# Optimization experiments

Hardware: AMD Instinct MI355X
Metric: run time of the kernel (lower is better)

The kernel has to match this reference:

```python
import jax, jax.numpy as jnp
import numpy as np

B, N, DIM = 2, 2048, 512
HEADS, DIM_HEAD = 8, 64
INNER = HEADS * DIM_HEAD  # 512
SCALE = DIM_HEAD ** -0.5


def setup_inputs() -> dict:
    key = jax.random.key(0)
    k1, k2, k3, k4, k5 = jax.random.split(key, 5)
    s = 0.02
    return {
        "x1": jax.random.normal(k1, (B, N, DIM), jnp.float32),
        "x2": jax.random.normal(k2, (B, N, DIM), jnp.float32),
        "W_qk": jax.random.normal(k3, (DIM, 2 * INNER), jnp.float32) * s,
        "W_v": jax.random.normal(k4, (DIM, INNER), jnp.float32) * s,
        "W_out": jax.random.normal(k5, (INNER, DIM), jnp.float32) * s,
        "b_out": jnp.zeros((DIM,), jnp.float32),
    }


def _split_heads(t):
    # [b, n, h*d] -> [b, h, n, d]
    b, n, _ = t.shape
    return t.reshape(b, n, HEADS, DIM_HEAD).transpose(0, 2, 1, 3)


def reference(x1, x2, W_qk, W_v, W_out, b_out):
    # to_qk(x1) -> chunk into k, v ; to_v(x2) -> q  (names in orig are swapped)
    kv = x1 @ W_qk                      # [b, n1, 2*inner]
    k, v = jnp.split(kv, 2, axis=-1)
    q = x2 @ W_v                        # [b, n2, inner]
    q, k, v = _split_heads(q), _split_heads(k), _split_heads(v)  # [b,h,n,d]
    dots = jnp.einsum("bhid,bhjd->bhij", q, k) * SCALE  # [b,h,n2,n1]
    attn = jax.nn.softmax(dots, axis=-1)
    out = jnp.einsum("bhij,bhjd->bhid", attn, v)         # [b,h,n2,d]
    out = out.transpose(0, 2, 1, 3).reshape(out.shape[0], out.shape[2], INNER)
    return out @ W_out + b_out          # [b, n2, dim]
```

## Files before the change

kernel.cpp:

```cpp
#include <hip/hip_runtime.h>

typedef short bf16x8 __attribute__((ext_vector_type(8)));
typedef short bf16x4 __attribute__((ext_vector_type(4)));
typedef float f32x4 __attribute__((ext_vector_type(4)));
typedef float f32x16 __attribute__((ext_vector_type(16)));
typedef unsigned short u16;
typedef u16 u16x8 __attribute__((ext_vector_type(8)));
typedef u16 u16x4 __attribute__((ext_vector_type(4)));

#define DEV __device__ __forceinline__

DEV u16 f2bf(float f) {
  unsigned u = __float_as_uint(f);
  u += 0x7fff + ((u >> 16) & 1);
  return (u16)(u >> 16);
}

DEV int pkbf(float lo, float hi) {
  return __builtin_amdgcn_perm(__float_as_uint(hi) + 0x8000u,
                               __float_as_uint(lo) + 0x8000u, 0x07060302u);
}

#define MFMA16(a, b, c) __builtin_amdgcn_mfma_f32_16x16x32_bf16(a, b, c, 0, 0, 0)
#define MFMA3216(a, b, c) __builtin_amdgcn_mfma_f32_32x32x16_bf16(a, b, c, 0, 0, 0)

#if __has_builtin(__builtin_amdgcn_mfma_f32_32x32x8bf16_1k)
#define HAVE_PV8 1
#define PVMFMA(a, b, c) __builtin_amdgcn_mfma_f32_32x32x8bf16_1k(a, b, c, 0, 0, 0)
#else
#define HAVE_PV8 0
#endif

__global__ __launch_bounds__(256) void wprep(
    const float* __restrict__ Wqk, const float* __restrict__ Wv,
    const float* __restrict__ Wout,
    u16* __restrict__ WqkT, u16* __restrict__ WvT, u16* __restrict__ WoutT) {
  __shared__ float tf[32][33];
  int bx = blockIdx.x, t = threadIdx.x;
  const float* src; u16* dst; int Ncols; int id;
  if (bx < 512)      { id = bx;       src = Wqk;  dst = WqkT;  Ncols = 1024; }
  else if (bx < 768) { id = bx - 512; src = Wv;   dst = WvT;   Ncols = 512; }
  else               { id = bx - 768; src = Wout; dst = WoutT; Ncols = 512; }
  int tilesPerRow = Ncols >> 5;
  int tr = id / tilesPerRow, tc = id % tilesPerRow;
  int r0 = tr * 32, c0 = tc * 32;
  {
    int r = t >> 3, c4 = (t & 7) * 4;
    float4 v = *(const float4*)(src + (long)(r0 + r) * Ncols + c0 + c4);
    tf[r][c4] = v.x; tf[r][c4 + 1] = v.y; tf[r][c4 + 2] = v.z; tf[r][c4 + 3] = v.w;
  }
  __syncthreads();
  {
    int c = t >> 3, r4 = (t & 7) * 4;
    u16x4 o;
    o[0] = f2bf(tf[r4][c]); o[1] = f2bf(tf[r4 + 1][c]);
    o[2] = f2bf(tf[r4 + 2][c]); o[3] = f2bf(tf[r4 + 3][c]);
    *(u16x4*)(dst + (long)(c0 + c) * 512 + r0 + r4) = o;
  }
}

template <int MODE>
__global__ __launch_bounds__(256) void gemm_k(
    const void* __restrict__ Ap, const u16* __restrict__ BT,
    u16* __restrict__ out_q, u16* __restrict__ out_k, u16* __restrict__ out_vt,
    float* __restrict__ out_f, const float* __restrict__ bias) {
  constexpr bool AF32 = (MODE != 2);
  __shared__ u16 sA[2][128 * 40];
  __shared__ u16 sB[2][64 * 40];
  int t = threadIdx.x, bx = blockIdx.x;
  int m0 = (bx & 31) * 128, n0 = (bx >> 5) * 64;
  int w = t >> 6, l = t & 63, lm = l & 15, lq = l >> 4;

  f32x4 zero = {0.f, 0.f, 0.f, 0.f};
  f32x4 acc[2][4];
#pragma unroll
  for (int i = 0; i < 2; ++i)
#pragma unroll
    for (int j = 0; j < 4; ++j) acc[i][j] = zero;

  int sm = t >> 2;
  int skc = (t & 3) * 8;
  const float* gAf = (const float*)Ap + (long)(m0 + sm) * 512 + skc;
  const u16* gAh = (const u16*)Ap + (long)(m0 + sm) * 512 + skc;
  const u16* gB = BT + (long)(n0 + sm) * 512 + skc;

  auto loadA = [&](int kt, int rows) {
    bf16x8 o;
    long off = (long)rows * 512 + kt * 32;
    if constexpr (AF32) {
      float4 f0 = *(const float4*)(gAf + off);
      float4 f1 = *(const float4*)(gAf + off + 4);
      o[0] = (short)f2bf(f0.x); o[1] = (short)f2bf(f0.y);
      o[2] = (short)f2bf(f0.z); o[3] = (short)f2bf(f0.w);
      o[4] = (short)f2bf(f1.x); o[5] = (short)f2bf(f1.y);
      o[6] = (short)f2bf(f1.z); o[7] = (short)f2bf(f1.w);
    } else {
      o = *(const bf16x8*)(gAh + off);
    }
    return o;
  };

  bf16x8 a0 = loadA(0, 0);
  bf16x8 a1 = loadA(0, 64);
  bf16x8 b0 = *(const bf16x8*)(gB);
  *(bf16x8*)(sA[0] + sm * 40 + skc) = a0;
  *(bf16x8*)(sA[0] + (sm + 64) * 40 + skc) = a1;
  *(bf16x8*)(sB[0] + sm * 40 + skc) = b0;
  __syncthreads();

  for (int kt = 0; kt < 16; ++kt) {
    int cur = kt & 1;
    if (kt < 15) {
      a0 = loadA(kt + 1, 0);
      a1 = loadA(kt + 1, 64);
      b0 = *(const bf16x8*)(gB + (kt + 1) * 32);
    }
    bf16x8 af[2], bfr[4];
    af[0] = *(const bf16x8*)(sA[cur] + (w * 32 + lm) * 40 + lq * 8);
    af[1] = *(const bf16x8*)(sA[cur] + (w * 32 + 16 + lm) * 40 + lq * 8);
#pragma unroll
    for (int s = 0; s < 4; ++s)
      bfr[s] = *(const bf16x8*)(sB[cur] + (s * 16 + lm) * 40 + lq * 8);
#pragma unroll
    for (int ms = 0; ms < 2; ++ms)
#pragma unroll
      for (int s = 0; s < 4; ++s)
        acc[ms][s] = MFMA16(af[ms], bfr[s], acc[ms][s]);
    if (kt < 15) {
      int nxt = 1 - cur;
      *(bf16x8*)(sA[nxt] + sm * 40 + skc) = a0;
      *(bf16x8*)(sA[nxt] + (sm + 64) * 40 + skc) = a1;
      *(bf16x8*)(sB[nxt] + sm * 40 + skc) = b0;
    }
    __syncthreads();
  }

#pragma unroll
  for (int ms = 0; ms < 2; ++ms) {
    int gmBase = m0 + w * 32 + ms * 16 + lq * 4;
#pragma unroll
    for (int s = 0; s < 4; ++s) {
      int gc = n0 + s * 16 + lm;
      if (MODE == 2) {
#pragma unroll
        for (int r = 0; r < 4; ++r)
          out_f[(long)(gmBase + r) * 512 + gc] = acc[ms][s][r] + bias[gc];
      } else if (MODE == 0) {
        int b = gmBase >> 11, n = gmBase & 2047;
#pragma unroll
        for (int r = 0; r < 4; ++r)
          out_q[(((long)(b << 3) + (gc >> 6)) * 2048 + n + r) * 64 + (gc & 63)] =
              f2bf(acc[ms][s][r] * 0.125f);
      } else {
        int b = gmBase >> 11, n = gmBase & 2047;
        if (gc < 512) {
#pragma unroll
          for (int r = 0; r < 4; ++r)
            out_k[(((long)(b << 3) + (gc >> 6)) * 2048 + n + r) * 64 + (gc & 63)] =
                f2bf(acc[ms][s][r]);
        } else {
          int c = gc - 512, h = c >> 6, d = c & 63;
          u16x4 vv;
#pragma unroll
          for (int r = 0; r < 4; ++r) vv[r] = f2bf(acc[ms][s][r]);
          *(u16x4*)(out_vt + (((long)(b << 3) + h) * 64 + d) * 2048 + n) = vv;
        }
      }
    }
  }
}

__global__ __launch_bounds__(128) void attn(
    const u16* __restrict__ Q, const u16* __restrict__ K,
    const u16* __restrict__ Vt, u16* __restrict__ O) {
  int id = blockIdx.x;
  int bh = id & 15, qt = id >> 4;
  int b = bh >> 3, h = bh & 7;
  const u16* Kh = K + (long)bh * 2048 * 64;
  const u16* Vh = Vt + (long)bh * 64 * 2048;
  int t = threadIdx.x, w = t >> 6, lane = t & 63, ln = lane & 31, hi = lane >> 5;

  __shared__ u16 sK[2][64 * 72];
  __shared__ u16 sV[2][64 * 72];

  bf16x8 qf[4];
  {
    const u16* qp = Q + (long)bh * 2048 * 64 + (long)(qt * 64 + w * 32 + ln) * 64 + hi * 8;
#pragma unroll
    for (int dc = 0; dc < 4; ++dc) qf[dc] = *(const bf16x8*)(qp + dc * 16);
  }

  f32x16 accO[2];
#pragma unroll
  for (int dt = 0; dt < 2; ++dt)
#pragma unroll
    for (int i = 0; i < 16; ++i) accO[dt][i] = 0.f;
  float dacc = 0.f;

  int r = t >> 1, half = t & 1;
  const u16* gK = Kh + (long)r * 64 + half * 32;
  const u16* gV = Vh + (long)r * 2048 + half * 32;
  int woff = r * 72 + half * 32;

  bf16x8 kp[4], vp[4];
#pragma unroll
  for (int i = 0; i < 4; ++i) {
    kp[i] = *(const bf16x8*)(gK + i * 8);
    vp[i] = *(const bf16x8*)(gV + i * 8);
  }
#pragma unroll
  for (int i = 0; i < 4; ++i) {
    *(bf16x8*)(sK[0] + woff + i * 8) = kp[i];
    *(bf16x8*)(sV[0] + woff + i * 8) = vp[i];
  }
  __syncthreads();

  for (int jt = 0; jt < 32; ++jt) {
    int cur = jt & 1;
    if (jt < 31) {
      long ko = (long)(jt + 1) * 64 * 64, vo = (long)(jt + 1) * 64;
#pragma unroll
      for (int i = 0; i < 4; ++i) {
        kp[i] = *(const bf16x8*)(gK + ko + i * 8);
        vp[i] = *(const bf16x8*)(gV + vo + i * 8);
      }
    }
    const u16* bK = sK[cur];
    const u16* bV = sV[cur];

#pragma unroll
    for (int kt2 = 0; kt2 < 2; ++kt2) {
      f32x16 st;
#pragma unroll
      for (int i = 0; i < 16; ++i) st[i] = 0.f;
#pragma unroll
      for (int dc = 0; dc < 4; ++dc) {
        bf16x8 kf = *(const bf16x8*)(bK + (kt2 * 32 + ln) * 72 + dc * 16 + hi * 8);
        st = MFMA3216(kf, qf[dc], st);
      }
      float p[16];
#pragma unroll
      for (int i = 0; i < 16; ++i) {
        float e = __expf(st[i]);
        p[i] = e;
        dacc += e;
      }
#if HAVE_PV8
#pragma unroll
      for (int c = 0; c < 4; ++c) {
        union { int2 i2; bf16x4 v; } u;
        u.i2.x = pkbf(p[c * 4 + 0], p[c * 4 + 1]);
        u.i2.y = pkbf(p[c * 4 + 2], p[c * 4 + 3]);
#pragma unroll
        for (int dt = 0; dt < 2; ++dt) {
          bf16x4 vf = *(const bf16x4*)(bV + (dt * 32 + ln) * 72 + kt2 * 32 + c * 8 + hi * 4);
          accO[dt] = PVMFMA(vf, u.v, accO[dt]);
        }
      }
#else
#pragma unroll
      for (int c2 = 0; c2 < 2; ++c2) {
        int o0x = pkbf(p[c2 * 8 + 0], p[c2 * 8 + 1]);
        int o0y = pkbf(p[c2 * 8 + 2], p[c2 * 8 + 3]);
        int o1x = pkbf(p[c2 * 8 + 4], p[c2 * 8 + 5]);
        int o1y = pkbf(p[c2 * 8 + 6], p[c2 * 8 + 7]);
        int s0x = __shfl_xor(o0x, 32), s0y = __shfl_xor(o0y, 32);
        int s1x = __shfl_xor(o1x, 32), s1y = __shfl_xor(o1y, 32);
        union { int4 i4; bf16x8 v; } u;
        if (hi) { u.i4.x = s1x; u.i4.y = s1y; u.i4.z = o1x; u.i4.w = o1y; }
        else    { u.i4.x = o0x; u.i4.y = o0y; u.i4.z = s0x; u.i4.w = s0y; }
#pragma unroll
        for (int dt = 0; dt < 2; ++dt) {
          bf16x8 vf = *(const bf16x8*)(bV + (dt * 32 + ln) * 72 + kt2 * 32 + c2 * 16 + hi * 8);
          accO[dt] = MFMA3216(vf, u.v, accO[dt]);
        }
      }
#endif
    }

    if (jt < 31) {
      int nxt = cur ^ 1;
#pragma unroll
      for (int i = 0; i < 4; ++i) {
        *(bf16x8*)(sK[nxt] + woff + i * 8) = kp[i];
        *(bf16x8*)(sV[nxt] + woff + i * 8) = vp[i];
      }
    }
    __syncthreads();
  }

  dacc += __shfl_xor(dacc, 32);
  float inv = 1.f / dacc;

  u16* Ob = O + ((long)b * 2048 + qt * 64 + w * 32 + ln) * 512 + h * 64;
#pragma unroll
  for (int dt = 0; dt < 2; ++dt)
#pragma unroll
    for (int g = 0; g < 4; ++g) {
      u16x4 o;
#pragma unroll
      for (int rr = 0; rr < 4; ++rr) o[rr] = f2bf(accO[dt][g * 4 + rr] * inv);
      *(u16x4*)(Ob + dt * 32 + g * 8 + hi * 4) = o;
    }
}

extern "C" void kernel_launch(void* const* d_in, const int* in_sizes, int n_in,
                              void* d_out, int out_size, void* d_ws, size_t ws_size,
                              hipStream_t stream) {
  const float* x1 = (const float*)d_in[0];
  const float* x2 = (const float*)d_in[1];
  const float* Wqk = (const float*)d_in[2];
  const float* Wv = (const float*)d_in[3];
  const float* Wout = (const float*)d_in[4];
  const float* bout = (const float*)d_in[5];
  float* out = (float*)d_out;

  u16* ws = (u16*)d_ws;
  const long SZ = 2097152;
  u16* Qw = ws;
  u16* Kw = ws + SZ;
  u16* Vtw = ws + 2 * SZ;
  u16* Ow = ws + 3 * SZ;
  u16* WqkT = ws + 4 * SZ;
  u16* WvT = WqkT + 524288;
  u16* WoutT = WvT + 262144;

  wprep<<<1024, 256, 0, stream>>>(Wqk, Wv, Wout, WqkT, WvT, WoutT);
  gemm_k<0><<<256, 256, 0, stream>>>(x2, WvT, Qw, nullptr, nullptr, nullptr, nullptr);
  gemm_k<1><<<512, 256, 0, stream>>>(x1, WqkT, nullptr, Kw, Vtw, nullptr, nullptr);
  attn<<<512, 128, 0, stream>>>(Qw, Kw, Vtw, Ow);
  gemm_k<2><<<256, 256, 0, stream>>>(Ow, WoutT, nullptr, nullptr, nullptr, out, bout);
}
```

Before: 145.3 us.

## Merge Q/KV projection launches, split attention keys across warps, shrink output GEMM tiles

```diff
diff --git a/kernel.cpp b/kernel.cpp
--- a/kernel.cpp
+++ b/kernel.cpp
@@ -59,16 +59,18 @@
   }
 }
 
-template <int MODE>
-__global__ __launch_bounds__(256) void gemm_k(
-    const void* __restrict__ Ap, const u16* __restrict__ BT,
-    u16* __restrict__ out_q, u16* __restrict__ out_k, u16* __restrict__ out_vt,
-    float* __restrict__ out_f, const float* __restrict__ bias) {
-  constexpr bool AF32 = (MODE != 2);
+__global__ __launch_bounds__(256) void qkv_gemm(
+    const float* __restrict__ x1, const float* __restrict__ x2,
+    const u16* __restrict__ WqkT, const u16* __restrict__ WvT,
+    u16* __restrict__ out_q, u16* __restrict__ out_k, u16* __restrict__ out_vt) {
   __shared__ u16 sA[2][128 * 40];
   __shared__ u16 sB[2][64 * 40];
-  int t = threadIdx.x, bx = blockIdx.x;
-  int m0 = (bx & 31) * 128, n0 = (bx >> 5) * 64;
+  int bx = blockIdx.x, t = threadIdx.x;
+  bool isQ = bx < 256;
+  int bx2 = isQ ? bx : bx - 256;
+  const float* Ap = isQ ? x2 : x1;
+  const u16* BT = isQ ? WvT : WqkT;
+  int m0 = (bx2 & 31) * 128, n0 = (bx2 >> 5) * 64;
   int w = t >> 6, l = t & 63, lm = l & 15, lq = l >> 4;
 
   f32x4 zero = {0.f, 0.f, 0.f, 0.f};
@@ -80,23 +82,18 @@
 
   int sm = t >> 2;
   int skc = (t & 3) * 8;
-  const float* gAf = (const float*)Ap + (long)(m0 + sm) * 512 + skc;
-  const u16* gAh = (const u16*)Ap + (long)(m0 + sm) * 512 + skc;
+  const float* gAf = Ap + (long)(m0 + sm) * 512 + skc;
   const u16* gB = BT + (long)(n0 + sm) * 512 + skc;
 
   auto loadA = [&](int kt, int rows) {
+    long off = (long)rows * 512 + kt * 32;
+    float4 f0 = *(const float4*)(gAf + off);
+    float4 f1 = *(const float4*)(gAf + off + 4);
     bf16x8 o;
-    long off = (long)rows * 512 + kt * 32;
-    if constexpr (AF32) {
-      float4 f0 = *(const float4*)(gAf + off);
-      float4 f1 = *(const float4*)(gAf + off + 4);
-      o[0] = (short)f2bf(f0.x); o[1] = (short)f2bf(f0.y);
-      o[2] = (short)f2bf(f0.z); o[3] = (short)f2bf(f0.w);
-      o[4] = (short)f2bf(f1.x); o[5] = (short)f2bf(f1.y);
-      o[6] = (short)f2bf(f1.z); o[7] = (short)f2bf(f1.w);
-    } else {
-      o = *(const bf16x8*)(gAh + off);
-    }
+    o[0] = (short)f2bf(f0.x); o[1] = (short)f2bf(f0.y);
+    o[2] = (short)f2bf(f0.z); o[3] = (short)f2bf(f0.w);
+    o[4] = (short)f2bf(f1.x); o[5] = (short)f2bf(f1.y);
+    o[6] = (short)f2bf(f1.z); o[7] = (short)f2bf(f1.w);
     return o;
   };
 
@@ -141,36 +138,29 @@
 #pragma unroll
     for (int s = 0; s < 4; ++s) {
       int gc = n0 + s * 16 + lm;
-      if (MODE == 2) {
-#pragma unroll
-        for (int r = 0; r < 4; ++r)
-          out_f[(long)(gmBase + r) * 512 + gc] = acc[ms][s][r] + bias[gc];
-      } else if (MODE == 0) {
-        int b = gmBase >> 11, n = gmBase & 2047;
+      int b = gmBase >> 11, n = gmBase & 2047;
+      if (isQ) {
 #pragma unroll
         for (int r = 0; r < 4; ++r)
           out_q[(((long)(b << 3) + (gc >> 6)) * 2048 + n + r) * 64 + (gc & 63)] =
               f2bf(acc[ms][s][r] * 0.125f);
+      } else if (gc < 512) {
+#pragma unroll
+        for (int r = 0; r < 4; ++r)
+          out_k[(((long)(b << 3) + (gc >> 6)) * 2048 + n + r) * 64 + (gc & 63)] =
+              f2bf(acc[ms][s][r]);
       } else {
-        int b = gmBase >> 11, n = gmBase & 2047;
-        if (gc < 512) {
-#pragma unroll
-          for (int r = 0; r < 4; ++r)
-            out_k[(((long)(b << 3) + (gc >> 6)) * 2048 + n + r) * 64 + (gc & 63)] =
-                f2bf(acc[ms][s][r]);
-        } else {
-          int c = gc - 512, h = c >> 6, d = c & 63;
-          u16x4 vv;
-#pragma unroll
-          for (int r = 0; r < 4; ++r) vv[r] = f2bf(acc[ms][s][r]);
-          *(u16x4*)(out_vt + (((long)(b << 3) + h) * 64 + d) * 2048 + n) = vv;
-        }
-      }
-    }
-  }
-}
-
-__global__ __launch_bounds__(128) void attn(
+        int c = gc - 512, h = c >> 6, d = c & 63;
+        u16x4 vv;
+#pragma unroll
+        for (int r = 0; r < 4; ++r) vv[r] = f2bf(acc[ms][s][r]);
+        *(u16x4*)(out_vt + (((long)(b << 3) + h) * 64 + d) * 2048 + n) = vv;
+      }
+    }
+  }
+}
+
+__global__ __launch_bounds__(256, 2) void attn(
     const u16* __restrict__ Q, const u16* __restrict__ K,
     const u16* __restrict__ Vt, u16* __restrict__ O) {
   int id = blockIdx.x;
@@ -179,27 +169,29 @@
   const u16* Kh = K + (long)bh * 2048 * 64;
   const u16* Vh = Vt + (long)bh * 64 * 2048;
   int t = threadIdx.x, w = t >> 6, lane = t & 63, ln = lane & 31, hi = lane >> 5;
-
-  __shared__ u16 sK[2][64 * 72];
-  __shared__ u16 sV[2][64 * 72];
+  int g = w & 1, kh = w >> 1;
+
+  __shared__ u16 sK[2][2][64 * 72];
+  __shared__ u16 sV[2][2][64 * 72];
 
   bf16x8 qf[4];
   {
-    const u16* qp = Q + (long)bh * 2048 * 64 + (long)(qt * 64 + w * 32 + ln) * 64 + hi * 8;
+    const u16* qp = Q + (long)bh * 2048 * 64 + (long)(qt * 64 + g * 32 + ln) * 64 + hi * 8;
 #pragma unroll
     for (int dc = 0; dc < 4; ++dc) qf[dc] = *(const bf16x8*)(qp + dc * 16);
   }
 
-  f32x16 accO[2];
+  f32x16 accOa[2], accOb[2];
 #pragma unroll
   for (int dt = 0; dt < 2; ++dt)
 #pragma unroll
-    for (int i = 0; i < 16; ++i) accO[dt][i] = 0.f;
+    for (int i = 0; i < 16; ++i) { accOa[dt][i] = 0.f; accOb[dt][i] = 0.f; }
   float dacc = 0.f;
 
-  int r = t >> 1, half = t & 1;
-  const u16* gK = Kh + (long)r * 64 + half * 32;
-  const u16* gV = Vh + (long)r * 2048 + half * 32;
+  int tp = t & 127;
+  int r = tp >> 1, half = tp & 1;
+  const u16* gK = Kh + (long)(kh * 1024 + r) * 64 + half * 32;
+  const u16* gV = Vh + (long)r * 2048 + kh * 1024 + half * 32;
   int woff = r * 72 + half * 32;
 
   bf16x8 kp[4], vp[4];
@@ -210,14 +202,14 @@
   }
 #pragma unroll
   for (int i = 0; i < 4; ++i) {
-    *(bf16x8*)(sK[0] + woff + i * 8) = kp[i];
-    *(bf16x8*)(sV[0] + woff + i * 8) = vp[i];
+    *(bf16x8*)(sK[kh][0] + woff + i * 8) = kp[i];
+    *(bf16x8*)(sV[kh][0] + woff + i * 8) = vp[i];
   }
   __syncthreads();
 
-  for (int jt = 0; jt < 32; ++jt) {
+  for (int jt = 0; jt < 16; ++jt) {
     int cur = jt & 1;
-    if (jt < 31) {
+    if (jt < 15) {
       long ko = (long)(jt + 1) * 64 * 64, vo = (long)(jt + 1) * 64;
 #pragma unroll
       for (int i = 0; i < 4; ++i) {
@@ -225,23 +217,26 @@
         vp[i] = *(const bf16x8*)(gV + vo + i * 8);
       }
     }
-    const u16* bK = sK[cur];
-    const u16* bV = sV[cur];
+    const u16* bK = sK[kh][cur];
+    const u16* bV = sV[kh][cur];
 
 #pragma unroll
     for (int kt2 = 0; kt2 < 2; ++kt2) {
-      f32x16 st;
-#pragma unroll
-      for (int i = 0; i < 16; ++i) st[i] = 0.f;
-#pragma unroll
-      for (int dc = 0; dc < 4; ++dc) {
-        bf16x8 kf = *(const bf16x8*)(bK + (kt2 * 32 + ln) * 72 + dc * 16 + hi * 8);
-        st = MFMA3216(kf, qf[dc], st);
-      }
+      f32x16 st1, st2;
+#pragma unroll
+      for (int i = 0; i < 16; ++i) { st1[i] = 0.f; st2[i] = 0.f; }
+      bf16x8 kf0 = *(const bf16x8*)(bK + (kt2 * 32 + ln) * 72 + 0 * 16 + hi * 8);
+      bf16x8 kf1 = *(const bf16x8*)(bK + (kt2 * 32 + ln) * 72 + 1 * 16 + hi * 8);
+      bf16x8 kf2 = *(const bf16x8*)(bK + (kt2 * 32 + ln) * 72 + 2 * 16 + hi * 8);
+      bf16x8 kf3 = *(const bf16x8*)(bK + (kt2 * 32 + ln) * 72 + 3 * 16 + hi * 8);
+      st1 = MFMA3216(kf0, qf[0], st1);
+      st2 = MFMA3216(kf1, qf[1], st2);
+      st1 = MFMA3216(kf2, qf[2], st1);
+      st2 = MFMA3216(kf3, qf[3], st2);
       float p[16];
 #pragma unroll
       for (int i = 0; i < 16; ++i) {
-        float e = __expf(st[i]);
+        float e = __expf(st1[i] + st2[i]);
         p[i] = e;
         dacc += e;
       }
@@ -254,7 +249,10 @@
 #pragma unroll
         for (int dt = 0; dt < 2; ++dt) {
           bf16x4 vf = *(const bf16x4*)(bV + (dt * 32 + ln) * 72 + kt2 * 32 + c * 8 + hi * 4);
-          accO[dt] = PVMFMA(vf, u.v, accO[dt]);
+          if (c & 1)
+            accOb[dt] = PVMFMA(vf, u.v, accOb[dt]);
+          else
+            accOa[dt] = PVMFMA(vf, u.v, accOa[dt]);
         }
       }
 #else
@@ -272,36 +270,133 @@
 #pragma unroll
         for (int dt = 0; dt < 2; ++dt) {
           bf16x8 vf = *(const bf16x8*)(bV + (dt * 32 + ln) * 72 + kt2 * 32 + c2 * 16 + hi * 8);
-          accO[dt] = MFMA3216(vf, u.v, accO[dt]);
+          if (c2 & 1)
+            accOb[dt] = MFMA3216(vf, u.v, accOb[dt]);
+          else
+            accOa[dt] = MFMA3216(vf, u.v, accOa[dt]);
         }
       }
 #endif
     }
 
-    if (jt < 31) {
+    if (jt < 15) {
       int nxt = cur ^ 1;
 #pragma unroll
       for (int i = 0; i < 4; ++i) {
-        *(bf16x8*)(sK[nxt] + woff + i * 8) = kp[i];
-        *(bf16x8*)(sV[nxt] + woff + i * 8) = vp[i];
+        *(bf16x8*)(sK[kh][nxt] + woff + i * 8) = kp[i];
+        *(bf16x8*)(sV[kh][nxt] + woff + i * 8) = vp[i];
       }
     }
     __syncthreads();
   }
 
-  dacc += __shfl_xor(dacc, 32);
-  float inv = 1.f / dacc;
-
-  u16* Ob = O + ((long)b * 2048 + qt * 64 + w * 32 + ln) * 512 + h * 64;
+  f32x16 accO[2];
 #pragma unroll
   for (int dt = 0; dt < 2; ++dt)
 #pragma unroll
-    for (int g = 0; g < 4; ++g) {
-      u16x4 o;
-#pragma unroll
-      for (int rr = 0; rr < 4; ++rr) o[rr] = f2bf(accO[dt][g * 4 + rr] * inv);
-      *(u16x4*)(Ob + dt * 32 + g * 8 + hi * 4) = o;
-    }
+    for (int i = 0; i < 16; ++i) accO[dt][i] = accOa[dt][i] + accOb[dt][i];
+
+  float* cb = (float*)&sK[0][0][0];
+  float* base = cb + g * 4224;
+  if (kh == 1) {
+#pragma unroll
+    for (int dt = 0; dt < 2; ++dt)
+#pragma unroll
+      for (int i = 0; i < 16; ++i)
+        base[(dt * 16 + i) * 64 + hi * 32 + ln] = accO[dt][i];
+    base[4096 + hi * 32 + ln] = dacc;
+  }
+  __syncthreads();
+  if (kh == 0) {
+#pragma unroll
+    for (int dt = 0; dt < 2; ++dt)
+#pragma unroll
+      for (int i = 0; i < 16; ++i)
+        accO[dt][i] += base[(dt * 16 + i) * 64 + hi * 32 + ln];
+    dacc += base[4096 + hi * 32 + ln];
+    dacc += __shfl_xor(dacc, 32);
+    float inv = 1.f / dacc;
+
+    u16* Ob = O + ((long)b * 2048 + qt * 64 + g * 32 + ln) * 512 + h * 64;
+#pragma unroll
+    for (int dt = 0; dt < 2; ++dt)
+#pragma unroll
+      for (int gq = 0; gq < 4; ++gq) {
+        u16x4 o;
+#pragma unroll
+        for (int rr = 0; rr < 4; ++rr) o[rr] = f2bf(accO[dt][gq * 4 + rr] * inv);
+        *(u16x4*)(Ob + dt * 32 + gq * 8 + hi * 4) = o;
+      }
+  }
+}
+
+__global__ __launch_bounds__(128) void out_gemm(
+    const u16* __restrict__ A, const u16* __restrict__ BT,
+    float* __restrict__ out_f, const float* __restrict__ bias) {
+  __shared__ u16 sA[2][64 * 40];
+  __shared__ u16 sB[2][32 * 40];
+  int t = threadIdx.x, bx = blockIdx.x;
+  int m0 = (bx & 63) * 64, n0 = (bx >> 6) * 32;
+  int w = t >> 6, l = t & 63, lm = l & 15, lq = l >> 4;
+
+  f32x4 zero = {0.f, 0.f, 0.f, 0.f};
+  f32x4 acc[2][2];
+#pragma unroll
+  for (int i = 0; i < 2; ++i)
+#pragma unroll
+    for (int j = 0; j < 2; ++j) acc[i][j] = zero;
+
+  int ar = t >> 1, akc = (t & 1) * 16;
+  int br = t >> 2, bkc = (t & 3) * 8;
+  const u16* gA = A + (long)(m0 + ar) * 512 + akc;
+  const u16* gB = BT + (long)(n0 + br) * 512 + bkc;
+
+  bf16x8 a0 = *(const bf16x8*)(gA);
+  bf16x8 a1 = *(const bf16x8*)(gA + 8);
+  bf16x8 b0 = *(const bf16x8*)(gB);
+  *(bf16x8*)(sA[0] + ar * 40 + akc) = a0;
+  *(bf16x8*)(sA[0] + ar * 40 + akc + 8) = a1;
+  *(bf16x8*)(sB[0] + br * 40 + bkc) = b0;
+  __syncthreads();
+
+  for (int kt = 0; kt < 16; ++kt) {
+    int cur = kt & 1;
+    if (kt < 15) {
+      a0 = *(const bf16x8*)(gA + (kt + 1) * 32);
+      a1 = *(const bf16x8*)(gA + (kt + 1) * 32 + 8);
+      b0 = *(const bf16x8*)(gB + (kt + 1) * 32);
+    }
+    bf16x8 af[2], bfr[2];
+    af[0] = *(const bf16x8*)(sA[cur] + (w * 32 + lm) * 40 + lq * 8);
+    af[1] = *(const bf16x8*)(sA[cur] + (w * 32 + 16 + lm) * 40 + lq * 8);
+    bfr[0] = *(const bf16x8*)(sB[cur] + (lm)*40 + lq * 8);
+    bfr[1] = *(const bf16x8*)(sB[cur] + (16 + lm) * 40 + lq * 8);
+#pragma unroll
+    for (int ms = 0; ms < 2; ++ms)
+#pragma unroll
+      for (int s = 0; s < 2; ++s)
+        acc[ms][s] = MFMA16(af[ms], bfr[s], acc[ms][s]);
+    if (kt < 15) {
+      int nxt = 1 - cur;
+      *(bf16x8*)(sA[nxt] + ar * 40 + akc) = a0;
+      *(bf16x8*)(sA[nxt] + ar * 40 + akc + 8) = a1;
+      *(bf16x8*)(sB[nxt] + br * 40 + bkc) = b0;
+    }
+    __syncthreads();
+  }
+
+#pragma unroll
+  for (int ms = 0; ms < 2; ++ms) {
+    int gmBase = m0 + w * 32 + ms * 16 + lq * 4;
+#pragma unroll
+    for (int s = 0; s < 2; ++s) {
+      int gc = n0 + s * 16 + lm;
+      float bv = bias[gc];
+#pragma unroll
+      for (int r = 0; r < 4; ++r)
+        out_f[(long)(gmBase + r) * 512 + gc] = acc[ms][s][r] + bv;
+    }
+  }
 }
 
 extern "C" void kernel_launch(void* const* d_in, const int* in_sizes, int n_in,
@@ -326,8 +421,7 @@
   u16* WoutT = WvT + 262144;
 
   wprep<<<1024, 256, 0, stream>>>(Wqk, Wv, Wout, WqkT, WvT, WoutT);
-  gemm_k<0><<<256, 256, 0, stream>>>(x2, WvT, Qw, nullptr, nullptr, nullptr, nullptr);
-  gemm_k<1><<<512, 256, 0, stream>>>(x1, WqkT, nullptr, Kw, Vtw, nullptr, nullptr);
-  attn<<<512, 128, 0, stream>>>(Qw, Kw, Vtw, Ow);
-  gemm_k<2><<<256, 256, 0, stream>>>(Ow, WoutT, nullptr, nullptr, nullptr, out, bout);
-}
+  qkv_gemm<<<768, 256, 0, stream>>>(x1, x2, WqkT, WvT, Qw, Kw, Vtw);
+  attn<<<512, 256, 0, stream>>>(Qw, Kw, Vtw, Ow);
+  out_gemm<<<1024, 128, 0, stream>>>(Ow, WoutT, out, bout);
+}
```

Measured after the change: 129.8 us. -10.6%, faster.
